# Optimization experiments

Measured on AMD Instinct MI355X. Metric: run time of the kernel, lower is better.

Reference implementation:

```python
import jax, jax.numpy as jnp
import numpy as np

ANCHORS = np.array([[10,13],[16,30],[33,23],[30,61],[62,45],[59,119],[116,90],[156,198],[373,326]], np.float32)
ANCHOR_MASK = [[6, 7, 8], [3, 4, 5], [0, 1, 2]]
INPUT_SHAPE = np.array([416, 416], np.float32)  # (h, w)
NUM_CLASSES = 80
EPS = 1e-7


def _bce(pred, target):
    # clip_by_tensor + binary cross entropy, as in the torch module
    p = jnp.clip(pred, EPS, 1.0 - EPS)
    return -target * jnp.log(p) - (1.0 - target) * jnp.log(1.0 - p)


def _box_iou(b1, b2):
    # b1: (..., 1, 4), b2: (..., n, 4), center-format xywh (normalized)
    b1_xy, b1_wh = b1[..., :2], b1[..., 2:4]
    b2_xy, b2_wh = b2[..., :2], b2[..., 2:4]
    b1_min, b1_max = b1_xy - b1_wh / 2.0, b1_xy + b1_wh / 2.0
    b2_min, b2_max = b2_xy - b2_wh / 2.0, b2_xy + b2_wh / 2.0
    inter_wh = jnp.maximum(jnp.minimum(b1_max, b2_max) - jnp.maximum(b1_min, b2_min), 0.0)
    inter = inter_wh[..., 0] * inter_wh[..., 1]
    a1 = b1_wh[..., 0] * b1_wh[..., 1]
    a2 = b2_wh[..., 0] * b2_wh[..., 1]
    return inter / (a1 + a2 - inter)


def _decode(y_pred, anchors):
    # y_pred: (b, 3*(5+C), h, w) -> raw: (b, 3, h, w, 5+C)
    b, _, h, w = y_pred.shape
    raw = y_pred.reshape(b, 3, 5 + NUM_CLASSES, h, w).transpose(0, 1, 3, 4, 2)
    gy, gx = jnp.meshgrid(jnp.arange(h, dtype=y_pred.dtype), jnp.arange(w, dtype=y_pred.dtype), indexing='ij')
    grid_xy = jnp.stack([gx, gy], axis=-1)  # (h, w, 2)
    pred_xy = jax.nn.sigmoid(raw[..., 0:2])
    pred_wh = raw[..., 2:4]                 # raw tw, th (MSE'd against log target)
    pred_conf = jax.nn.sigmoid(raw[..., 4:5])
    pred_class = jax.nn.sigmoid(raw[..., 5:])
    # decoded, normalized boxes for IoU-based negative mining
    box_xy = (pred_xy + grid_xy) / jnp.array([w, h], y_pred.dtype)
    box_wh = jnp.exp(pred_wh) * anchors.reshape(3, 1, 1, 2) / jnp.asarray(INPUT_SHAPE[::-1].copy())
    pred_box = jnp.concatenate([box_xy, box_wh], axis=-1)  # (b,3,h,w,4)
    return grid_xy, pred_box, pred_xy, pred_wh, pred_conf, pred_class


def _layer_loss(y_pred, y_true, target, anchors):
    b, _, h, w = y_pred.shape
    grid_xy, pred_box, pred_xy, pred_wh, pred_conf, pred_class = _decode(y_pred, anchors)
    object_mask = y_true[..., 4:5]
    true_xy = y_true[..., 0:2] * jnp.array([h, w], y_pred.dtype) - grid_xy
    true_wh = jnp.log(y_true[..., 2:4] * jnp.asarray(INPUT_SHAPE[::-1].copy()) / anchors.reshape(3, 1, 1, 2))
    true_wh = jnp.where(object_mask > 0, true_wh, jnp.zeros_like(true_wh))
    loss_scale = 2.0 - y_true[..., 2:3] * y_true[..., 3:4]
    # negative mask: every grid/anchor prediction vs all true boxes of its image (vectorized over batch)
    iou = _box_iou(pred_box[:, :, :, :, None, :], target[:, None, None, None, :, :4])  # (b,3,h,w,n)
    best_iou = jnp.max(iou, axis=-1)
    neg = (best_iou < 0.5).astype(y_pred.dtype)[..., None]
    neg_mask = (1.0 - object_mask) * neg
    loss_xy = jnp.sum(object_mask * loss_scale * _bce(pred_xy, true_xy))
    loss_wh = jnp.sum(object_mask * loss_scale * 0.5 * (pred_wh - true_wh) ** 2)
    conf_bce = _bce(pred_conf, object_mask)
    loss_conf = jnp.sum(object_mask * conf_bce) + jnp.sum(neg_mask * conf_bce)
    loss_cls = jnp.sum(object_mask * _bce(pred_class, y_true[..., 5:]))
    return loss_xy + loss_wh + loss_conf + loss_cls


def setup_inputs() -> dict:
    key = jax.random.key(0)
    ks = jax.random.split(key, 7)
    grids = [13, 26, 52]
    b, n = 32, 20
    inp = {}
    for i, g in enumerate(grids):
        inp[f'y_pred{i}'] = jax.random.normal(ks[i], (b, 3 * (5 + NUM_CLASSES), g, g), jnp.float32)
        # y_true values in (0.05, 0.95): keeps log(true_wh) and 1/y_true grads bounded
        inp[f'y_true{i}'] = 0.05 + 0.9 * jax.random.uniform(ks[3 + i], (b, 3, g, g, 5 + NUM_CLASSES), jnp.float32)
    inp['target'] = 0.05 + 0.9 * jax.random.uniform(ks[6], (b, n, 5), jnp.float32)
    return inp


def reference(y_pred0, y_pred1, y_pred2, y_true0, y_true1, y_true2, target):
    total = jnp.zeros((), jnp.float32)
    for yp, yt, mask in ((y_pred0, y_true0, ANCHOR_MASK[0]),
                         (y_pred1, y_true1, ANCHOR_MASK[1]),
                         (y_pred2, y_true2, ANCHOR_MASK[2])):
        total = total + _layer_loss(yp, yt, target, jnp.asarray(ANCHORS[mask]))
    return total
```

## Files before the change

kernel.cpp:

```cpp
#include <hip/hip_runtime.h>
#include <math.h>

#define BLOCK 256
#define NB0 64
#define NB1 254
#define NB2 1014
#define NBLOCKS (NB0 + NB1 + NB2)

typedef float f4a __attribute__((ext_vector_type(4), aligned(4)));

__constant__ float c_anch[9][2] = {
    {116.f, 90.f}, {156.f, 198.f}, {373.f, 326.f},
    { 30.f, 61.f}, { 62.f,  45.f}, { 59.f, 119.f},
    { 10.f, 13.f}, { 16.f,  30.f}, { 33.f,  23.f}
};

__device__ __forceinline__ float softplusf(float x) {
    float ax = fabsf(x);
    return fmaxf(x, 0.f) + __logf(1.f + __expf(-ax));
}

__device__ __forceinline__ float sigmoidf(float x) {
    return __fdividef(1.f, 1.f + __expf(-x));
}


template<int Q>
__device__ __forceinline__ void stage_cls(const float* __restrict__ tw, int lane,
                                          int nvc, bool full, float* r) {
    if (full) {
        int lo = (lane >> 4) * 85 + (lane & 15);
#pragma unroll
        for (int k = 0; k < 16; k++)
            r[k] = tw[lo + k * 340 + 5 + Q * 16];
    } else {
#pragma unroll
        for (int k = 0; k < 16; k++) {
            int cc = min(k * 4 + (lane >> 4), nvc - 1);
            r[k] = tw[cc * 85 + (lane & 15) + 5 + Q * 16];
        }
    }
}

__device__ __forceinline__ void write_cls(float (*S)[17], int lane, const float* r) {
#pragma unroll
    for (int k = 0; k < 16; k++)
        S[k * 4 + (lane >> 4)][lane & 15] = r[k];
}

template<int Q>
__device__ __forceinline__ float consume_cls(const float (*S)[17],
                                             const float* __restrict__ pb,
                                             int lane, int hw) {
    float cls = 0.f;
#pragma unroll
    for (int c = 0; c < 16; c++) {
        float x = pb[(size_t)((5 + Q * 16 + c) * hw)];
        float t = S[lane][c];
        cls += softplusf(x) - t * x;
    }
    return cls;
}

__global__ __launch_bounds__(BLOCK, 6) void yolo_loss_main(
    const float* __restrict__ p0, const float* __restrict__ p1, const float* __restrict__ p2,
    const float* __restrict__ t0, const float* __restrict__ t1, const float* __restrict__ t2,
    const float* __restrict__ tgt, float* __restrict__ partials)
{
    __shared__ float sh[4][64][17];

    int blk = blockIdx.x;
    const float* pred;
    const float* tru;
    int layer, g, cells, bbase;
    if (blk < NB0)            { layer = 0; pred = p0; tru = t0; g = 13; cells = 16224;  bbase = 0; }
    else if (blk < NB0 + NB1) { layer = 1; pred = p1; tru = t1; g = 26; cells = 64896;  bbase = NB0; }
    else                      { layer = 2; pred = p2; tru = t2; g = 52; cells = 259584; bbase = NB0 + NB1; }

    int tid = threadIdx.x;
    int lane = tid & 63;
    int wv = tid >> 6;
    int cell0 = (blk - bbase) * BLOCK + wv * 64;
    int nv = cells - cell0;
    float acc = 0.f;

    if (nv > 0) {
        float (*S)[17] = sh[wv];
        bool full = (nv >= 64);
        int nvc = full ? 64 : nv;
        bool active = lane < nv;
        const float* tw = tru + (size_t)cell0 * 85;

        int cidx = active ? (cell0 + lane) : (cells - 1);
        int hw = g * g;
        int ij = cidx % hw;
        int a  = (cidx / hw) % 3;
        int b  = cidx / (3 * hw);
        int i  = ij / g;
        int j  = ij - i * g;
        const float* pb = pred + (size_t)((b * 3 + a) * 85) * hw + ij;

        {
            float hreg[5];
#pragma unroll
            for (int k = 0; k < 5; k++) {
                int f = k * 64 + lane;
                int cell = f / 5;
                int ch = f - cell * 5;
                int cc = full ? cell : min(cell, nvc - 1);
                hreg[k] = tw[cc * 85 + ch];
            }
#pragma unroll
            for (int k = 0; k < 5; k++) {
                int f = k * 64 + lane;
                int cell = f / 5;
                int ch = f - cell * 5;
                S[cell][ch] = hreg[k];
            }
        }

        float creg[16];
        stage_cls<0>(tw, lane, nvc, full, creg);

        float cls = 0.f, mask = 0.f;
        if (active) {
            float y0 = S[lane][0], y1 = S[lane][1], y2 = S[lane][2], y3 = S[lane][3];
            mask = S[lane][4];

            float r0 = pb[0];
            float r1 = pb[hw];
            float r2 = pb[2 * hw];
            float r3 = pb[3 * hw];
            float r4 = pb[4 * hw];

            float gf = (float)g, gx = (float)j, gy = (float)i;
            float aw = c_anch[layer * 3 + a][0];
            float ah = c_anch[layer * 3 + a][1];

            float true_x = y0 * gf - gx;
            float true_y = y1 * gf - gy;
            float ls = 2.f - y2 * y3;
            float lxy = (softplusf(r0) - true_x * r0) + (softplusf(r1) - true_y * r1);
            acc += mask * ls * lxy;

            float tw_ = __logf(y2 * (416.f / aw));
            float th_ = __logf(y3 * (416.f / ah));
            float dw = r2 - tw_, dh = r3 - th_;
            acc += mask * ls * 0.5f * (dw * dw + dh * dh);

            float cbce = softplusf(r4) - mask * r4;

            float sx = sigmoidf(r0);
            float sy = sigmoidf(r1);
            float bx = __fdividef(sx + gx, gf);
            float by = __fdividef(sy + gy, gf);
            float bw = __expf(r2) * aw * (1.f / 416.f);
            float bh = __expf(r3) * ah * (1.f / 416.f);
            float a1 = bw * bh;
            float b1minx = bx - 0.5f * bw, b1maxx = bx + 0.5f * bw;
            float b1miny = by - 0.5f * bh, b1maxy = by + 0.5f * bh;

            const float* tg = tgt + b * 20 * 5;
            float best = 0.f;
#pragma unroll 5
            for (int k = 0; k < 20; k++) {
                f4a t = *reinterpret_cast<const f4a*>(tg + k * 5);
                float hw2 = 0.5f * t.z, hh2 = 0.5f * t.w;
                float iw = fminf(b1maxx, t.x + hw2) - fmaxf(b1minx, t.x - hw2);
                float ih = fminf(b1maxy, t.y + hh2) - fmaxf(b1miny, t.y - hh2);
                iw = fmaxf(iw, 0.f);
                ih = fmaxf(ih, 0.f);
                float inter = iw * ih;
                float iou = __fdividef(inter, a1 + t.z * t.w - inter);
                best = fmaxf(best, iou);
            }
            float neg = (best < 0.5f) ? 1.f : 0.f;
            acc += mask * cbce + (1.f - mask) * neg * cbce;
        }

        write_cls(S, lane, creg);
        stage_cls<1>(tw, lane, nvc, full, creg);
        if (active) cls += consume_cls<0>(S, pb, lane, hw);

        write_cls(S, lane, creg);
        stage_cls<2>(tw, lane, nvc, full, creg);
        if (active) cls += consume_cls<1>(S, pb, lane, hw);

        write_cls(S, lane, creg);
        stage_cls<3>(tw, lane, nvc, full, creg);
        if (active) cls += consume_cls<2>(S, pb, lane, hw);

        write_cls(S, lane, creg);
        stage_cls<4>(tw, lane, nvc, full, creg);
        if (active) cls += consume_cls<3>(S, pb, lane, hw);

        write_cls(S, lane, creg);
        if (active) {
            cls += consume_cls<4>(S, pb, lane, hw);
            acc += mask * cls;
        }
    }

    for (int off = 32; off > 0; off >>= 1)
        acc += __shfl_down(acc, off, 64);
    __shared__ float shr[BLOCK / 64];
    if ((threadIdx.x & 63) == 0)
        shr[threadIdx.x >> 6] = acc;
    __syncthreads();
    if (threadIdx.x == 0) {
        float s = 0.f;
        for (int w = 0; w < BLOCK / 64; w++) s += shr[w];
        partials[blockIdx.x] = s;
    }
}

__global__ __launch_bounds__(BLOCK) void yolo_loss_reduce(
    const float* __restrict__ partials, float* __restrict__ out)
{
    float s = 0.f;
    for (int i = threadIdx.x; i < NBLOCKS; i += BLOCK)
        s += partials[i];
    for (int off = 32; off > 0; off >>= 1)
        s += __shfl_down(s, off, 64);
    __shared__ float sh[BLOCK / 64];
    if ((threadIdx.x & 63) == 0)
        sh[threadIdx.x >> 6] = s;
    __syncthreads();
    if (threadIdx.x == 0) {
        float tot = 0.f;
        for (int wv = 0; wv < BLOCK / 64; wv++) tot += sh[wv];
        out[0] = tot;
    }
}

extern "C" void kernel_launch(void* const* d_in, const int* in_sizes, int n_in,
                              void* d_out, int out_size, void* d_ws, size_t ws_size,
                              hipStream_t stream) {
    const float* p0  = (const float*)d_in[0];
    const float* t0  = (const float*)d_in[1];
    const float* p1  = (const float*)d_in[2];
    const float* t1  = (const float*)d_in[3];
    const float* p2  = (const float*)d_in[4];
    const float* t2  = (const float*)d_in[5];
    const float* tgt = (const float*)d_in[6];
    float* partials  = (float*)d_ws;

    yolo_loss_main<<<NBLOCKS, BLOCK, 0, stream>>>(p0, p1, p2, t0, t1, t2, tgt, partials);
    yolo_loss_reduce<<<1, BLOCK, 0, stream>>>(partials, (float*)d_out);
}
```

Before: 253.1 us.

## Double-buffer class-channel loads with inline asm and prefetch ahead of header work

After: 253.6 us. No clear change (+0.2%).

```diff
diff --git a/kernel.cpp b/kernel.cpp
--- a/kernel.cpp
+++ b/kernel.cpp
@@ -25,44 +25,93 @@
 }
 
 
-template<int Q>
-__device__ __forceinline__ void stage_cls(const float* __restrict__ tw, int lane,
-                                          int nvc, bool full, float* r) {
-    if (full) {
-        int lo = (lane >> 4) * 85 + (lane & 15);
-#pragma unroll
-        for (int k = 0; k < 16; k++)
-            r[k] = tw[lo + k * 340 + 5 + Q * 16];
-    } else {
-#pragma unroll
-        for (int k = 0; k < 16; k++) {
-            int cc = min(k * 4 + (lane >> 4), nvc - 1);
-            r[k] = tw[cc * 85 + (lane & 15) + 5 + Q * 16];
-        }
-    }
-}
-
-__device__ __forceinline__ void write_cls(float (*S)[17], int lane, const float* r) {
+__device__ __forceinline__ void issue_pred16(const float* __restrict__ pred,
+                                             unsigned voff, unsigned shw4,
+                                             float (&x)[16]) {
+    asm volatile(
+        "global_load_dword %0, %16, %18\n\t"  "v_add_u32 %16, %17, %16\n\t"
+        "global_load_dword %1, %16, %18\n\t"  "v_add_u32 %16, %17, %16\n\t"
+        "global_load_dword %2, %16, %18\n\t"  "v_add_u32 %16, %17, %16\n\t"
+        "global_load_dword %3, %16, %18\n\t"  "v_add_u32 %16, %17, %16\n\t"
+        "global_load_dword %4, %16, %18\n\t"  "v_add_u32 %16, %17, %16\n\t"
+        "global_load_dword %5, %16, %18\n\t"  "v_add_u32 %16, %17, %16\n\t"
+        "global_load_dword %6, %16, %18\n\t"  "v_add_u32 %16, %17, %16\n\t"
+        "global_load_dword %7, %16, %18\n\t"  "v_add_u32 %16, %17, %16\n\t"
+        "global_load_dword %8, %16, %18\n\t"  "v_add_u32 %16, %17, %16\n\t"
+        "global_load_dword %9, %16, %18\n\t"  "v_add_u32 %16, %17, %16\n\t"
+        "global_load_dword %10, %16, %18\n\t" "v_add_u32 %16, %17, %16\n\t"
+        "global_load_dword %11, %16, %18\n\t" "v_add_u32 %16, %17, %16\n\t"
+        "global_load_dword %12, %16, %18\n\t" "v_add_u32 %16, %17, %16\n\t"
+        "global_load_dword %13, %16, %18\n\t" "v_add_u32 %16, %17, %16\n\t"
+        "global_load_dword %14, %16, %18\n\t" "v_add_u32 %16, %17, %16\n\t"
+        "global_load_dword %15, %16, %18"
+        : "=v"(x[0]), "=v"(x[1]), "=v"(x[2]), "=v"(x[3]),
+          "=v"(x[4]), "=v"(x[5]), "=v"(x[6]), "=v"(x[7]),
+          "=v"(x[8]), "=v"(x[9]), "=v"(x[10]), "=v"(x[11]),
+          "=v"(x[12]), "=v"(x[13]), "=v"(x[14]), "=v"(x[15]),
+          "+v"(voff)
+        : "s"(shw4), "s"(pred));
+}
+
+__device__ __forceinline__ void issue_true16(const float* __restrict__ tru,
+                                             unsigned voff, float (&c)[16]) {
+    asm volatile(
+        "global_load_dword %0, %16, %17\n\t"  "v_add_u32 %16, 1360, %16\n\t"
+        "global_load_dword %1, %16, %17\n\t"  "v_add_u32 %16, 1360, %16\n\t"
+        "global_load_dword %2, %16, %17\n\t"  "v_add_u32 %16, 1360, %16\n\t"
+        "global_load_dword %3, %16, %17\n\t"  "v_add_u32 %16, 1360, %16\n\t"
+        "global_load_dword %4, %16, %17\n\t"  "v_add_u32 %16, 1360, %16\n\t"
+        "global_load_dword %5, %16, %17\n\t"  "v_add_u32 %16, 1360, %16\n\t"
+        "global_load_dword %6, %16, %17\n\t"  "v_add_u32 %16, 1360, %16\n\t"
+        "global_load_dword %7, %16, %17\n\t"  "v_add_u32 %16, 1360, %16\n\t"
+        "global_load_dword %8, %16, %17\n\t"  "v_add_u32 %16, 1360, %16\n\t"
+        "global_load_dword %9, %16, %17\n\t"  "v_add_u32 %16, 1360, %16\n\t"
+        "global_load_dword %10, %16, %17\n\t" "v_add_u32 %16, 1360, %16\n\t"
+        "global_load_dword %11, %16, %17\n\t" "v_add_u32 %16, 1360, %16\n\t"
+        "global_load_dword %12, %16, %17\n\t" "v_add_u32 %16, 1360, %16\n\t"
+        "global_load_dword %13, %16, %17\n\t" "v_add_u32 %16, 1360, %16\n\t"
+        "global_load_dword %14, %16, %17\n\t" "v_add_u32 %16, 1360, %16\n\t"
+        "global_load_dword %15, %16, %17"
+        : "=v"(c[0]), "=v"(c[1]), "=v"(c[2]), "=v"(c[3]),
+          "=v"(c[4]), "=v"(c[5]), "=v"(c[6]), "=v"(c[7]),
+          "=v"(c[8]), "=v"(c[9]), "=v"(c[10]), "=v"(c[11]),
+          "=v"(c[12]), "=v"(c[13]), "=v"(c[14]), "=v"(c[15]),
+          "+v"(voff)
+        : "s"(tru));
+}
+
+__device__ __forceinline__ void write_cls(float (*S)[17], int lane, const float (&r)[16]) {
 #pragma unroll
     for (int k = 0; k < 16; k++)
         S[k * 4 + (lane >> 4)][lane & 15] = r[k];
 }
 
 template<int Q>
-__device__ __forceinline__ float consume_cls(const float (*S)[17],
-                                             const float* __restrict__ pb,
-                                             int lane, int hw) {
-    float cls = 0.f;
+__device__ __forceinline__ void class_phase_asm(
+    const float* __restrict__ pred, const float* __restrict__ tru,
+    float (*S)[17], int lane, unsigned pboff4, unsigned shw4, unsigned tbase4,
+    float (&xcur)[16], float (&xnext)[16],
+    float (&ccur)[16], float (&cnext)[16], float& cls)
+{
+    if constexpr (Q < 4) {
+        issue_pred16(pred, pboff4 + (unsigned)(5 + 16 * (Q + 1)) * shw4, shw4, xnext);
+        issue_true16(tru, tbase4 + (unsigned)(5 + 16 * (Q + 1)) * 4u, cnext);
+        asm volatile("s_waitcnt vmcnt(32)");
+    } else {
+        asm volatile("s_waitcnt vmcnt(0)");
+    }
+    __builtin_amdgcn_sched_barrier(0);
+    write_cls(S, lane, ccur);
 #pragma unroll
     for (int c = 0; c < 16; c++) {
-        float x = pb[(size_t)((5 + Q * 16 + c) * hw)];
         float t = S[lane][c];
-        cls += softplusf(x) - t * x;
-    }
-    return cls;
-}
-
-__global__ __launch_bounds__(BLOCK, 6) void yolo_loss_main(
+        cls += softplusf(xcur[c]) - t * xcur[c];
+    }
+    __builtin_amdgcn_sched_barrier(0);
+    (void)cnext;
+}
+
+__global__ __launch_bounds__(BLOCK, 4) void yolo_loss_main(
     const float* __restrict__ p0, const float* __restrict__ p1, const float* __restrict__ p2,
     const float* __restrict__ t0, const float* __restrict__ t1, const float* __restrict__ t2,
     const float* __restrict__ tgt, float* __restrict__ partials)
@@ -82,123 +131,171 @@
     int wv = tid >> 6;
     int cell0 = (blk - bbase) * BLOCK + wv * 64;
     int nv = cells - cell0;
+    int hw = g * g;
     float acc = 0.f;
 
-    if (nv > 0) {
+    if (nv >= 64) {
         float (*S)[17] = sh[wv];
-        bool full = (nv >= 64);
-        int nvc = full ? 64 : nv;
-        bool active = lane < nv;
         const float* tw = tru + (size_t)cell0 * 85;
 
-        int cidx = active ? (cell0 + lane) : (cells - 1);
-        int hw = g * g;
+        int cidx = cell0 + lane;
         int ij = cidx % hw;
         int a  = (cidx / hw) % 3;
         int b  = cidx / (3 * hw);
         int i  = ij / g;
         int j  = ij - i * g;
-        const float* pb = pred + (size_t)((b * 3 + a) * 85) * hw + ij;
-
-        {
-            float hreg[5];
+        int pbo = ((b * 3 + a) * 85) * hw + ij;
+        const float* pb = pred + (size_t)pbo;
+
+        unsigned shw4   = (unsigned)hw * 4u;
+        unsigned pboff4 = (unsigned)pbo * 4u;
+        unsigned tbase4 = (unsigned)((cell0 + (lane >> 4)) * 85 + (lane & 15)) * 4u;
+
+        float xA[16], xB[16], cA[16], cB[16];
+
+        issue_pred16(pred, pboff4 + 5u * shw4, shw4, xA);
+        issue_true16(tru, tbase4 + 20u, cA);
+
+        float hreg[5];
 #pragma unroll
-            for (int k = 0; k < 5; k++) {
-                int f = k * 64 + lane;
-                int cell = f / 5;
-                int ch = f - cell * 5;
-                int cc = full ? cell : min(cell, nvc - 1);
-                hreg[k] = tw[cc * 85 + ch];
-            }
+        for (int k = 0; k < 5; k++) {
+            int f = k * 64 + lane;
+            int cell = f / 5;
+            int ch = f - cell * 5;
+            hreg[k] = tw[cell * 85 + ch];
+        }
 #pragma unroll
-            for (int k = 0; k < 5; k++) {
-                int f = k * 64 + lane;
-                int cell = f / 5;
-                int ch = f - cell * 5;
-                S[cell][ch] = hreg[k];
-            }
-        }
-
-        float creg[16];
-        stage_cls<0>(tw, lane, nvc, full, creg);
-
-        float cls = 0.f, mask = 0.f;
-        if (active) {
-            float y0 = S[lane][0], y1 = S[lane][1], y2 = S[lane][2], y3 = S[lane][3];
-            mask = S[lane][4];
-
-            float r0 = pb[0];
-            float r1 = pb[hw];
-            float r2 = pb[2 * hw];
-            float r3 = pb[3 * hw];
-            float r4 = pb[4 * hw];
-
-            float gf = (float)g, gx = (float)j, gy = (float)i;
-            float aw = c_anch[layer * 3 + a][0];
-            float ah = c_anch[layer * 3 + a][1];
-
-            float true_x = y0 * gf - gx;
-            float true_y = y1 * gf - gy;
-            float ls = 2.f - y2 * y3;
-            float lxy = (softplusf(r0) - true_x * r0) + (softplusf(r1) - true_y * r1);
-            acc += mask * ls * lxy;
-
-            float tw_ = __logf(y2 * (416.f / aw));
-            float th_ = __logf(y3 * (416.f / ah));
-            float dw = r2 - tw_, dh = r3 - th_;
-            acc += mask * ls * 0.5f * (dw * dw + dh * dh);
-
-            float cbce = softplusf(r4) - mask * r4;
-
-            float sx = sigmoidf(r0);
-            float sy = sigmoidf(r1);
-            float bx = __fdividef(sx + gx, gf);
-            float by = __fdividef(sy + gy, gf);
-            float bw = __expf(r2) * aw * (1.f / 416.f);
-            float bh = __expf(r3) * ah * (1.f / 416.f);
-            float a1 = bw * bh;
-            float b1minx = bx - 0.5f * bw, b1maxx = bx + 0.5f * bw;
-            float b1miny = by - 0.5f * bh, b1maxy = by + 0.5f * bh;
-
-            const float* tg = tgt + b * 20 * 5;
-            float best = 0.f;
+        for (int k = 0; k < 5; k++) {
+            int f = k * 64 + lane;
+            int cell = f / 5;
+            int ch = f - cell * 5;
+            S[cell][ch] = hreg[k];
+        }
+
+        float y0 = S[lane][0], y1 = S[lane][1], y2 = S[lane][2], y3 = S[lane][3];
+        float mask = S[lane][4];
+
+        float r0 = pb[0];
+        float r1 = pb[hw];
+        float r2 = pb[2 * hw];
+        float r3 = pb[3 * hw];
+        float r4 = pb[4 * hw];
+
+        float gf = (float)g, gx = (float)j, gy = (float)i;
+        float aw = c_anch[layer * 3 + a][0];
+        float ah = c_anch[layer * 3 + a][1];
+
+        float true_x = y0 * gf - gx;
+        float true_y = y1 * gf - gy;
+        float ls = 2.f - y2 * y3;
+        float lxy = (softplusf(r0) - true_x * r0) + (softplusf(r1) - true_y * r1);
+        acc += mask * ls * lxy;
+
+        float tw_ = __logf(y2 * (416.f / aw));
+        float th_ = __logf(y3 * (416.f / ah));
+        float dw = r2 - tw_, dh = r3 - th_;
+        acc += mask * ls * 0.5f * (dw * dw + dh * dh);
+
+        float cbce = softplusf(r4) - mask * r4;
+
+        float sx = sigmoidf(r0);
+        float sy = sigmoidf(r1);
+        float bx = __fdividef(sx + gx, gf);
+        float by = __fdividef(sy + gy, gf);
+        float bw = __expf(r2) * aw * (1.f / 416.f);
+        float bh = __expf(r3) * ah * (1.f / 416.f);
+        float a1 = bw * bh;
+        float b1minx = bx - 0.5f * bw, b1maxx = bx + 0.5f * bw;
+        float b1miny = by - 0.5f * bh, b1maxy = by + 0.5f * bh;
+
+        const float* tg = tgt + b * 20 * 5;
+        float best = 0.f;
 #pragma unroll 5
-            for (int k = 0; k < 20; k++) {
-                f4a t = *reinterpret_cast<const f4a*>(tg + k * 5);
-                float hw2 = 0.5f * t.z, hh2 = 0.5f * t.w;
-                float iw = fminf(b1maxx, t.x + hw2) - fmaxf(b1minx, t.x - hw2);
-                float ih = fminf(b1maxy, t.y + hh2) - fmaxf(b1miny, t.y - hh2);
-                iw = fmaxf(iw, 0.f);
-                ih = fmaxf(ih, 0.f);
-                float inter = iw * ih;
-                float iou = __fdividef(inter, a1 + t.z * t.w - inter);
-                best = fmaxf(best, iou);
-            }
-            float neg = (best < 0.5f) ? 1.f : 0.f;
-            acc += mask * cbce + (1.f - mask) * neg * cbce;
-        }
-
-        write_cls(S, lane, creg);
-        stage_cls<1>(tw, lane, nvc, full, creg);
-        if (active) cls += consume_cls<0>(S, pb, lane, hw);
-
-        write_cls(S, lane, creg);
-        stage_cls<2>(tw, lane, nvc, full, creg);
-        if (active) cls += consume_cls<1>(S, pb, lane, hw);
-
-        write_cls(S, lane, creg);
-        stage_cls<3>(tw, lane, nvc, full, creg);
-        if (active) cls += consume_cls<2>(S, pb, lane, hw);
-
-        write_cls(S, lane, creg);
-        stage_cls<4>(tw, lane, nvc, full, creg);
-        if (active) cls += consume_cls<3>(S, pb, lane, hw);
-
-        write_cls(S, lane, creg);
-        if (active) {
-            cls += consume_cls<4>(S, pb, lane, hw);
-            acc += mask * cls;
-        }
+        for (int k = 0; k < 20; k++) {
+            f4a t = *reinterpret_cast<const f4a*>(tg + k * 5);
+            float hw2 = 0.5f * t.z, hh2 = 0.5f * t.w;
+            float iw = fminf(b1maxx, t.x + hw2) - fmaxf(b1minx, t.x - hw2);
+            float ih = fminf(b1maxy, t.y + hh2) - fmaxf(b1miny, t.y - hh2);
+            iw = fmaxf(iw, 0.f);
+            ih = fmaxf(ih, 0.f);
+            float inter = iw * ih;
+            float iou = __fdividef(inter, a1 + t.z * t.w - inter);
+            best = fmaxf(best, iou);
+        }
+        float neg = (best < 0.5f) ? 1.f : 0.f;
+        acc += mask * cbce + (1.f - mask) * neg * cbce;
+
+        float cls = 0.f;
+        class_phase_asm<0>(pred, tru, S, lane, pboff4, shw4, tbase4, xA, xB, cA, cB, cls);
+        class_phase_asm<1>(pred, tru, S, lane, pboff4, shw4, tbase4, xB, xA, cB, cA, cls);
+        class_phase_asm<2>(pred, tru, S, lane, pboff4, shw4, tbase4, xA, xB, cA, cB, cls);
+        class_phase_asm<3>(pred, tru, S, lane, pboff4, shw4, tbase4, xB, xA, cB, cA, cls);
+        class_phase_asm<4>(pred, tru, S, lane, pboff4, shw4, tbase4, xA, xB, cA, cB, cls);
+
+        acc += mask * cls;
+    } else if (nv > 0 && lane < nv) {
+        int cidx = cell0 + lane;
+        int ij = cidx % hw;
+        int a  = (cidx / hw) % 3;
+        int b  = cidx / (3 * hw);
+        int i  = ij / g;
+        int j  = ij - i * g;
+        const float* pb = pred + (size_t)(((b * 3 + a) * 85) * hw + ij);
+        const float* tb = tru + (size_t)cidx * 85;
+
+        float y0 = tb[0], y1 = tb[1], y2 = tb[2], y3 = tb[3], mask = tb[4];
+        float r0 = pb[0], r1 = pb[hw], r2 = pb[2 * hw], r3 = pb[3 * hw], r4 = pb[4 * hw];
+
+        float gf = (float)g, gx = (float)j, gy = (float)i;
+        float aw = c_anch[layer * 3 + a][0];
+        float ah = c_anch[layer * 3 + a][1];
+
+        float true_x = y0 * gf - gx;
+        float true_y = y1 * gf - gy;
+        float ls = 2.f - y2 * y3;
+        float lxy = (softplusf(r0) - true_x * r0) + (softplusf(r1) - true_y * r1);
+        acc += mask * ls * lxy;
+
+        float tw_ = __logf(y2 * (416.f / aw));
+        float th_ = __logf(y3 * (416.f / ah));
+        float dw = r2 - tw_, dh = r3 - th_;
+        acc += mask * ls * 0.5f * (dw * dw + dh * dh);
+
+        float cbce = softplusf(r4) - mask * r4;
+
+        float sx = sigmoidf(r0);
+        float sy = sigmoidf(r1);
+        float bx = __fdividef(sx + gx, gf);
+        float by = __fdividef(sy + gy, gf);
+        float bw = __expf(r2) * aw * (1.f / 416.f);
+        float bh = __expf(r3) * ah * (1.f / 416.f);
+        float a1 = bw * bh;
+        float b1minx = bx - 0.5f * bw, b1maxx = bx + 0.5f * bw;
+        float b1miny = by - 0.5f * bh, b1maxy = by + 0.5f * bh;
+
+        const float* tg = tgt + b * 20 * 5;
+        float best = 0.f;
+        for (int k = 0; k < 20; k++) {
+            f4a t = *reinterpret_cast<const f4a*>(tg + k * 5);
+            float hw2 = 0.5f * t.z, hh2 = 0.5f * t.w;
+            float iw = fminf(b1maxx, t.x + hw2) - fmaxf(b1minx, t.x - hw2);
+            float ih = fminf(b1maxy, t.y + hh2) - fmaxf(b1miny, t.y - hh2);
+            iw = fmaxf(iw, 0.f);
+            ih = fmaxf(ih, 0.f);
+            float inter = iw * ih;
+            float iou = __fdividef(inter, a1 + t.z * t.w - inter);
+            best = fmaxf(best, iou);
+        }
+        float neg = (best < 0.5f) ? 1.f : 0.f;
+        acc += mask * cbce + (1.f - mask) * neg * cbce;
+
+        float cls = 0.f;
+        for (int c = 0; c < 80; c++) {
+            float x = pb[(size_t)(5 + c) * hw];
+            float t = tb[5 + c];
+            cls += softplusf(x) - t * x;
+        }
+        acc += mask * cls;
     }
 
     for (int off = 32; off > 0; off >>= 1)
```
